# Kernel optimization log

Hardware: AMD Instinct MI355X
Metric: run time of the kernel (lower is better)

The kernel has to match this reference:

```python
import jax, jax.numpy as jnp
import numpy as np

NUM_CLASSES = 2
THRESHOLD = 0.5
NEGPOS_RATIO = 3
VAR0, VAR1 = 0.1, 0.2  # self.variance = [0.1, 0.2]


def point_form(priors):
    # [cx,cy,w,h] -> [xmin,ymin,xmax,ymax]
    return jnp.concatenate([priors[:, :2] - priors[:, 2:] / 2,
                            priors[:, :2] + priors[:, 2:] / 2], axis=1)


def jaccard(a, b):
    # a: [O,4], b: [P,4] point-form -> IoU [O,P]
    tl = jnp.maximum(a[:, None, :2], b[None, :, :2])
    br = jnp.minimum(a[:, None, 2:], b[None, :, 2:])
    wh = jnp.clip(br - tl, 0.0)
    inter = wh[..., 0] * wh[..., 1]
    area_a = ((a[:, 2] - a[:, 0]) * (a[:, 3] - a[:, 1]))[:, None]
    area_b = ((b[:, 2] - b[:, 0]) * (b[:, 3] - b[:, 1]))[None, :]
    return inter / (area_a + area_b - inter)


def encode(matched, priors):
    # matched: [P,4] point-form GT, priors: [P,4] center-size
    g_cxcy = ((matched[:, :2] + matched[:, 2:]) / 2 - priors[:, :2]) / (VAR0 * priors[:, 2:])
    g_wh = jnp.log((matched[:, 2:] - matched[:, :2]) / priors[:, 2:]) / VAR1
    return jnp.concatenate([g_cxcy, g_wh], axis=1)


def match_one(truths, labels, priors):
    # truths: [O,4], labels: [O], priors: [P,4]
    O = truths.shape[0]
    overlaps = jaccard(truths, point_form(priors))          # [O,P]
    best_prior_idx = jnp.argmax(overlaps, axis=1)           # [O] best prior per GT
    best_truth_overlap = jnp.max(overlaps, axis=0)          # [P]
    best_truth_idx = jnp.argmax(overlaps, axis=0)           # [P]
    # ensure each GT keeps its best prior
    best_truth_overlap = best_truth_overlap.at[best_prior_idx].set(2.0)
    best_truth_idx = best_truth_idx.at[best_prior_idx].set(jnp.arange(O))
    matches = truths[best_truth_idx]                        # [P,4]
    conf = labels[best_truth_idx].astype(jnp.int32)         # head label == 1
    conf = jnp.where(best_truth_overlap < THRESHOLD, 0, conf)
    loc = encode(matches, priors)                           # [P,4]
    return loc, conf


def setup_inputs() -> dict:
    key = jax.random.key(0)
    k1, k2, k3, k4, k5, k6 = jax.random.split(key, 6)
    B, P, O = 32, 32768, 32
    loc_data = jax.random.normal(k1, (B, P, 3), jnp.float32) * 0.1
    conf_data = jax.random.normal(k2, (B, P, 2), jnp.float32)
    cxy = jax.random.uniform(k3, (P, 2), jnp.float32, 0.1, 0.9)
    wh = jax.random.uniform(k4, (P, 2), jnp.float32, 0.05, 0.2)
    priors = jnp.concatenate([cxy, wh], axis=1)
    xy1 = jax.random.uniform(k5, (B, O, 2), jnp.float32, 0.0, 0.7)
    twh = jax.random.uniform(k6, (B, O, 2), jnp.float32, 0.05, 0.25)
    targets = jnp.concatenate([xy1, xy1 + twh, jnp.ones((B, O, 1), jnp.float32)], axis=2)
    return {"loc_data": loc_data, "conf_data": conf_data, "priors": priors, "targets": targets}


def reference(loc_data, conf_data, priors, targets):
    B, P, _ = loc_data.shape
    # convert_coord: [cx, cy, gw] -> [cx, cy, gw, gw]
    quard = jnp.stack([loc_data[..., 0], loc_data[..., 1],
                       loc_data[..., 2], loc_data[..., 2]], axis=-1)  # [B,P,4]
    truths = targets[..., :4]
    labels = targets[..., 4]
    loc_t, conf_t = jax.vmap(lambda t, l: match_one(t, l, priors))(truths, labels)
    pos = conf_t > 0                                         # [B,P]
    # localization smooth-L1 over positives (sum reduction)
    d = quard - loc_t
    ad = jnp.abs(d)
    sl1 = jnp.where(ad < 1.0, 0.5 * d * d, ad - 0.5)
    loss_l = jnp.sum(sl1 * pos[..., None].astype(sl1.dtype))
    # per-prior CE for hard-negative mining
    lse = jax.nn.logsumexp(conf_data, axis=-1)               # [B,P]
    picked = jnp.take_along_axis(conf_data, conf_t[..., None], axis=-1)[..., 0]
    ce = lse - picked                                        # [B,P]
    ce_mine = jnp.where(pos, 0.0, ce)
    # double argsort -> rank of each prior by mining loss (descending)
    loss_idx = jnp.argsort(-ce_mine, axis=1)
    idx_rank = jnp.argsort(loss_idx, axis=1)
    num_pos = jnp.sum(pos.astype(jnp.int32), axis=1, keepdims=True)  # [B,1]
    num_neg = jnp.minimum(NEGPOS_RATIO * num_pos, P - 1)
    neg = idx_rank < num_neg
    sel = jnp.logical_or(pos, neg)
    loss_c = jnp.sum(jnp.where(sel, ce, 0.0))
    N = jnp.sum(num_pos).astype(loss_l.dtype)
    return loss_l / N, loss_c / N
```

## Files before the change

### kernel.cpp

```cpp
#include <hip/hip_runtime.h>
#include <math.h>

#define Bn 32
#define Pn 32768
#define On 32
#define TPB 256
#define PPT 2
#define BP  (TPB * PPT)
#define AG 8
#define AC 1024


__device__ __forceinline__ unsigned long long shfl_down_u64(unsigned long long v, int off) {
    unsigned lo = (unsigned)(v & 0xFFFFFFFFull);
    unsigned hi = (unsigned)(v >> 32);
    lo = __shfl_down(lo, off, 64);
    hi = __shfl_down(hi, off, 64);
    return ((unsigned long long)hi << 32) | lo;
}

__global__ __launch_bounds__(256) void matchA(const float4* __restrict__ priors,
                                              const float* __restrict__ targets,
                                              unsigned long long* __restrict__ bpm) {
    int g    = blockIdx.x;
    int base = blockIdx.y * AC;
    int tid  = threadIdx.x;

    __shared__ float4 tb[AG];
    __shared__ float  ta[AG];
    __shared__ unsigned long long sbest[AG];

    if (tid < AG) {
        const float* t = targets + (size_t)(g * AG + tid) * 5;
        float x1 = t[0], y1 = t[1], x2 = t[2], y2 = t[3];
        tb[tid] = make_float4(x1, y1, x2, y2);
        ta[tid] = (x2 - x1) * (y2 - y1);
        sbest[tid] = 0ull;
    }
    __syncthreads();

    float px1[4], py1[4], px2[4], py2[4], ab[4];
#pragma unroll
    for (int j = 0; j < 4; j++) {
        float4 pr = priors[base + tid + 256 * j];
        px1[j] = pr.x - pr.z * 0.5f; py1[j] = pr.y - pr.w * 0.5f;
        px2[j] = pr.x + pr.z * 0.5f; py2[j] = pr.y + pr.w * 0.5f;
        ab[j]  = (px2[j] - px1[j]) * (py2[j] - py1[j]);
    }

#pragma unroll
    for (int o = 0; o < AG; o++) {
        float4 tt = tb[o];
        float  a  = ta[o];
        float bI = 0.f, bU = 1.f;
        int   bj = 0;
#pragma unroll
        for (int j = 0; j < 4; j++) {
            float ix1 = fmaxf(tt.x, px1[j]), iy1 = fmaxf(tt.y, py1[j]);
            float ix2 = fminf(tt.z, px2[j]), iy2 = fminf(tt.w, py2[j]);
            float iw = fmaxf(ix2 - ix1, 0.f), ih = fmaxf(iy2 - iy1, 0.f);
            float I = iw * ih;
            float U = a + ab[j] - I;
            if (I * bU > bI * U) { bI = I; bU = U; bj = j; }
        }
        int p = base + tid + 256 * bj;
        float iou = bI / bU;
        unsigned long long key = ((unsigned long long)__float_as_uint(iou) << 32)
                               | (unsigned)(Pn - 1 - p);
#pragma unroll
        for (int off = 32; off > 0; off >>= 1) {
            unsigned long long other = shfl_down_u64(key, off);
            if (other > key) key = other;
        }
        if ((tid & 63) == 0) atomicMax(&sbest[o], key);
    }
    __syncthreads();
    if (tid < AG) atomicMax(&bpm[g * AG + tid], sbest[tid]);
}

__global__ __launch_bounds__(256) void matchB(const float* __restrict__ loc,
                                              const float2* __restrict__ conf2,
                                              const float4* __restrict__ priors,
                                              const float* __restrict__ targets,
                                              const unsigned long long* __restrict__ bpm,
                                              float* __restrict__ ce_mine,
                                              int* __restrict__ num_pos,
                                              float* __restrict__ loss_l_t,
                                              float* __restrict__ ce_t,
                                              int* __restrict__ np_tot) {
    int b = blockIdx.y;
    int base = blockIdx.x * BP;
    int tid = threadIdx.x;

    __shared__ float4 tb[On];
    __shared__ float  ta[On], lb[On];
    __shared__ int    forced[BP];
    __shared__ float  sred[12];

#pragma unroll
    for (int j = 0; j < PPT; j++) forced[tid + 256 * j] = -1;
    int sp = -1;
    if (tid < On) {
        const float* t = targets + ((size_t)b * On + tid) * 5;
        float x1 = t[0], y1 = t[1], x2 = t[2], y2 = t[3];
        tb[tid] = make_float4(x1, y1, x2, y2);
        ta[tid] = (x2 - x1) * (y2 - y1);
        lb[tid] = t[4];
        sp = Pn - 1 - (int)(bpm[b * On + tid] & 0xFFFFFFFFull);
    }
    __syncthreads();
    if (tid < On && sp >= base && sp < base + BP)
        atomicMax(&forced[sp - base], tid);
    __syncthreads();

    float px1[PPT], py1[PPT], px2[PPT], py2[PPT], ab[PPT], pcx[PPT], pcy[PPT], pw[PPT], ph[PPT];
#pragma unroll
    for (int j = 0; j < PPT; j++) {
        float4 pr = priors[base + tid + 256 * j];
        pcx[j] = pr.x; pcy[j] = pr.y; pw[j] = pr.z; ph[j] = pr.w;
        px1[j] = pr.x - pr.z * 0.5f; py1[j] = pr.y - pr.w * 0.5f;
        px2[j] = pr.x + pr.z * 0.5f; py2[j] = pr.y + pr.w * 0.5f;
        ab[j]  = (px2[j] - px1[j]) * (py2[j] - py1[j]);
    }

    float bI[PPT] = {0.f, 0.f};
    float bU[PPT] = {1.f, 1.f};
    int   bx[PPT] = {0, 0};
#pragma unroll 4
    for (int o = 0; o < On; o++) {
        float4 tt = tb[o];
        float  a  = ta[o];
#pragma unroll
        for (int j = 0; j < PPT; j++) {
            float ix1 = fmaxf(tt.x, px1[j]), iy1 = fmaxf(tt.y, py1[j]);
            float ix2 = fminf(tt.z, px2[j]), iy2 = fminf(tt.w, py2[j]);
            float iw = fmaxf(ix2 - ix1, 0.f), ih = fmaxf(iy2 - iy1, 0.f);
            float I = iw * ih;
            float U = a + ab[j] - I;
            if (I * bU[j] > bI[j] * U) { bI[j] = I; bU[j] = U; bx[j] = o; }
        }
    }

    float ll_s = 0.f, pce_s = 0.f, cnt_s = 0.f;
#pragma unroll
    for (int j = 0; j < PPT; j++) {
        int p = base + tid + 256 * j;
        int fo = forced[tid + 256 * j];
        int bidx = (fo >= 0) ? fo : bx[j];
        int cf;
        if (fo >= 0)                      cf = (int)lb[bidx];
        else if (bI[j] >= 0.5f * bU[j])   cf = (int)lb[bidx];
        else                              cf = 0;
        bool pos = cf > 0;

        if (pos) {
            float4 tt = tb[bidx];
            float g0 = ((tt.x + tt.z) * 0.5f - pcx[j]) / (0.1f * pw[j]);
            float g1 = ((tt.y + tt.w) * 0.5f - pcy[j]) / (0.1f * ph[j]);
            float g2 = __logf((tt.z - tt.x) / pw[j]) * 5.0f;
            float g3 = __logf((tt.w - tt.y) / ph[j]) * 5.0f;
            const float* lp = loc + ((size_t)b * Pn + p) * 3;
            float q0 = lp[0], q1 = lp[1], q2 = lp[2];
            float dd[4] = { q0 - g0, q1 - g1, q2 - g2, q2 - g3 };
#pragma unroll
            for (int i = 0; i < 4; i++) {
                float ad = fabsf(dd[i]);
                ll_s += (ad < 1.f) ? 0.5f * dd[i] * dd[i] : (ad - 0.5f);
            }
            cnt_s += 1.f;
        }

        float2 cc = conf2[(size_t)b * Pn + p];
        float m = fmaxf(cc.x, cc.y);
        float lse = m + __logf(__expf(cc.x - m) + __expf(cc.y - m));
        float ce = lse - (cf ? cc.y : cc.x);
        if (pos) { pce_s += ce; ce = 0.f; }
        ce_mine[(size_t)b * Pn + p] = fmaxf(ce, 0.f);
    }

#pragma unroll
    for (int off = 32; off > 0; off >>= 1) {
        ll_s  += __shfl_down(ll_s,  off, 64);
        pce_s += __shfl_down(pce_s, off, 64);
        cnt_s += __shfl_down(cnt_s, off, 64);
    }
    int lane = tid & 63, wv = tid >> 6;
    if (lane == 0) { sred[wv * 3] = ll_s; sred[wv * 3 + 1] = pce_s; sred[wv * 3 + 2] = cnt_s; }
    __syncthreads();
    if (tid == 0) {
        float llr = 0, pcer = 0, cntr = 0;
        for (int w = 0; w < 4; w++) { llr += sred[w*3]; pcer += sred[w*3+1]; cntr += sred[w*3+2]; }
        if (llr != 0.f)  atomicAdd(loss_l_t, llr);
        if (pcer != 0.f) atomicAdd(ce_t, pcer);
        int c = (int)cntr;
        if (c) { atomicAdd(&num_pos[b], c); atomicAdd(np_tot, c); }
    }
}

__global__ __launch_bounds__(1024) void topk(const float* __restrict__ ce_mine,
                                             const int* __restrict__ num_pos,
                                             float* __restrict__ ce_t) {
    int b = blockIdx.x, tid = threadIdx.x;
    const float4* v4 = (const float4*)(ce_mine + (size_t)b * Pn);
    float4 r[8];
#pragma unroll
    for (int i = 0; i < 8; i++) r[i] = v4[i * 1024 + tid];

    int k = 3 * num_pos[b];
    if (k > Pn - 1) k = Pn - 1;
    if (k <= 0) return;

    __shared__ int hist[4][2048];
    __shared__ int wavetot[16];
    __shared__ int waveabove[16];
    __shared__ unsigned long long wcand[16];
    __shared__ unsigned s_lo;
    __shared__ int s_ab;
    __shared__ float ssum[16];
    __shared__ int   scnt[16];

    int lane = tid & 63, wv = tid >> 6;
    unsigned LO = 0u;
    int AB = 0;

    const int shifts[3] = {20, 9, 0};
    const int nbs[3]    = {2048, 2048, 512};

#pragma unroll
    for (int rd = 0; rd < 3; rd++) {
        int shift = shifts[rd], nb = nbs[rd];
        int* hf = &hist[0][0];
        for (int i = tid; i < 4 * 2048; i += 1024) hf[i] = 0;
        __syncthreads();
        int* myh = hist[wv >> 2];
#pragma unroll
        for (int i = 0; i < 8; i++) {
            float4 rv = r[i];
            float vals[4] = {rv.x, rv.y, rv.z, rv.w};
#pragma unroll
            for (int q = 0; q < 4; q++) {
                unsigned u = __float_as_uint(vals[q]);
                unsigned bin = (u - LO) >> shift;
                if (bin < (unsigned)nb) atomicAdd(&myh[bin], 1);
            }
        }
        __syncthreads();
        int c0 = hist[0][2*tid] + hist[1][2*tid] + hist[2][2*tid] + hist[3][2*tid];
        int c1 = hist[0][2*tid+1] + hist[1][2*tid+1] + hist[2][2*tid+1] + hist[3][2*tid+1];
        int local = c0 + c1;
        int suf = local;
#pragma unroll
        for (int off = 1; off < 64; off <<= 1) {
            int src = lane + off;
            int o = __shfl(suf, src & 63, 64);
            suf += (src < 64) ? o : 0;
        }
        if (lane == 0) wavetot[wv] = suf;
        __syncthreads();
        if (tid == 0) {
            int acc = AB;
            for (int w = 15; w >= 0; w--) { waveabove[w] = acc; acc += wavetot[w]; }
        }
        __syncthreads();
        int S0 = waveabove[wv] + suf;
        int S1 = S0 - c0;
        int cand = -1; unsigned nab = 0;
        if (S0 >= k) { cand = 2*tid;     nab = (unsigned)(S0 - c0); }
        if (S1 >= k) { cand = 2*tid + 1; nab = (unsigned)(S1 - c1); }
        unsigned long long pk = ((unsigned long long)(unsigned)(cand + 1) << 32) | nab;
#pragma unroll
        for (int off = 32; off > 0; off >>= 1) {
            unsigned long long o = shfl_down_u64(pk, off);
            if (o > pk) pk = o;
        }
        if (lane == 0) wcand[wv] = pk;
        __syncthreads();
        if (tid == 0) {
            unsigned long long best = 0;
            for (int w = 0; w < 16; w++) if (wcand[w] > best) best = wcand[w];
            int ci = (int)(best >> 32) - 1;
            s_lo = LO + ((unsigned)ci << shift);
            s_ab = (int)(best & 0xFFFFFFFFu);
        }
        __syncthreads();
        LO = s_lo; AB = s_ab;
    }
    float tau = __uint_as_float(LO);
    float s = 0.f; int c = 0;
#pragma unroll
    for (int i = 0; i < 8; i++) {
        if (r[i].x > tau) { s += r[i].x; c++; }
        if (r[i].y > tau) { s += r[i].y; c++; }
        if (r[i].z > tau) { s += r[i].z; c++; }
        if (r[i].w > tau) { s += r[i].w; c++; }
    }
#pragma unroll
    for (int off = 32; off > 0; off >>= 1) {
        s += __shfl_down(s, off, 64);
        c += __shfl_down(c, off, 64);
    }
    if (lane == 0) { ssum[wv] = s; scnt[wv] = c; }
    __syncthreads();
    if (tid == 0) {
        float st = 0.f; int ct = 0;
        for (int w = 0; w < 16; w++) { st += ssum[w]; ct += scnt[w]; }
        atomicAdd(ce_t, st + (float)(k - ct) * tau);
    }
}

__global__ void finalize(const float* __restrict__ loss_l_t,
                         const float* __restrict__ ce_t,
                         const int* __restrict__ np_tot,
                         float* __restrict__ out) {
    float N = (float)(*np_tot);
    out[0] = *loss_l_t / N;
    out[1] = *ce_t / N;
}

extern "C" void kernel_launch(void* const* d_in, const int* in_sizes, int n_in,
                              void* d_out, int out_size, void* d_ws, size_t ws_size,
                              hipStream_t stream) {
    const float* loc     = (const float*)d_in[0];
    const float* conf    = (const float*)d_in[1];
    const float* priors  = (const float*)d_in[2];
    const float* targets = (const float*)d_in[3];
    float* out = (float*)d_out;

    char* ws = (char*)d_ws;
    unsigned long long* bpm = (unsigned long long*)ws;
    int*   num_pos  = (int*)(ws + 8192);
    float* loss_l_t = (float*)(ws + 8320);
    float* ce_t     = (float*)(ws + 8324);
    int*   np_tot   = (int*)(ws + 8328);
    float* ce_mine  = (float*)(ws + 16384);

    hipMemsetAsync(ws, 0, 16384, stream);

    hipLaunchKernelGGL(matchA, dim3((Bn * On) / AG, Pn / AC), dim3(256), 0, stream,
                       (const float4*)priors, targets, bpm);
    hipLaunchKernelGGL(matchB, dim3(Pn / BP, Bn), dim3(256), 0, stream,
                       loc, (const float2*)conf, (const float4*)priors, targets, bpm,
                       ce_mine, num_pos, loss_l_t, ce_t, np_tot);
    hipLaunchKernelGGL(topk, dim3(Bn), dim3(1024), 0, stream, ce_mine, num_pos, ce_t);
    hipLaunchKernelGGL(finalize, dim3(1), dim3(1), 0, stream, loss_l_t, ce_t, np_tot, out);
}
```

Before: 195.2 us.

## Fuse finalize into topk via last-block ticket, widen matchB per-thread work

The separate finalize launch is removed. The last topk block to finish now computes the outputs, using an atomic ticket counter and a threadfence. matchB goes from 2 to 4 priors per thread, so it launches half as many blocks. Its confidence loads are issued early to overlap with the IoU loop, and the IoU scan over ground-truth boxes is split into two independent argmax chains to shorten the dependency chain, merged afterwards. The wider per-thread work raises register pressure, and halving the grid may reduce occupancy.

```diff
diff --git a/kernel.cpp b/kernel.cpp
--- a/kernel.cpp
+++ b/kernel.cpp
@@ -5,7 +5,7 @@
 #define Pn 32768
 #define On 32
 #define TPB 256
-#define PPT 2
+#define PPT 4
 #define BP  (TPB * PPT)
 #define AG 8
 #define AC 1024
@@ -92,6 +92,10 @@
     int base = blockIdx.x * BP;
     int tid = threadIdx.x;
 
+    float2 cc[PPT];
+#pragma unroll
+    for (int j = 0; j < PPT; j++) cc[j] = conf2[(size_t)b * Pn + base + tid + 256 * j];
+
     __shared__ float4 tb[On];
     __shared__ float  ta[On], lb[On];
     __shared__ int    forced[BP];
@@ -123,22 +127,37 @@
         ab[j]  = (px2[j] - px1[j]) * (py2[j] - py1[j]);
     }
 
-    float bI[PPT] = {0.f, 0.f};
-    float bU[PPT] = {1.f, 1.f};
-    int   bx[PPT] = {0, 0};
-#pragma unroll 4
-    for (int o = 0; o < On; o++) {
-        float4 tt = tb[o];
-        float  a  = ta[o];
-#pragma unroll
-        for (int j = 0; j < PPT; j++) {
-            float ix1 = fmaxf(tt.x, px1[j]), iy1 = fmaxf(tt.y, py1[j]);
-            float ix2 = fminf(tt.z, px2[j]), iy2 = fminf(tt.w, py2[j]);
-            float iw = fmaxf(ix2 - ix1, 0.f), ih = fmaxf(iy2 - iy1, 0.f);
-            float I = iw * ih;
-            float U = a + ab[j] - I;
-            if (I * bU[j] > bI[j] * U) { bI[j] = I; bU[j] = U; bx[j] = o; }
-        }
+    float bIc[PPT][2], bUc[PPT][2];
+    int   bxc[PPT][2];
+#pragma unroll
+    for (int j = 0; j < PPT; j++)
+#pragma unroll
+        for (int h = 0; h < 2; h++) { bIc[j][h] = 0.f; bUc[j][h] = 1.f; bxc[j][h] = h * 16; }
+
+#pragma unroll 2
+    for (int o16 = 0; o16 < 16; o16++) {
+#pragma unroll
+        for (int h = 0; h < 2; h++) {
+            int o = h * 16 + o16;
+            float4 tt = tb[o];
+            float  a  = ta[o];
+#pragma unroll
+            for (int j = 0; j < PPT; j++) {
+                float ix1 = fmaxf(tt.x, px1[j]), iy1 = fmaxf(tt.y, py1[j]);
+                float ix2 = fminf(tt.z, px2[j]), iy2 = fminf(tt.w, py2[j]);
+                float iw = fmaxf(ix2 - ix1, 0.f), ih = fmaxf(iy2 - iy1, 0.f);
+                float I = iw * ih;
+                float U = a + ab[j] - I;
+                if (I * bUc[j][h] > bIc[j][h] * U) { bIc[j][h] = I; bUc[j][h] = U; bxc[j][h] = o; }
+            }
+        }
+    }
+    float bI[PPT], bU[PPT];
+    int   bx[PPT];
+#pragma unroll
+    for (int j = 0; j < PPT; j++) {
+        bI[j] = bIc[j][0]; bU[j] = bUc[j][0]; bx[j] = bxc[j][0];
+        if (bIc[j][1] * bU[j] > bI[j] * bUc[j][1]) { bI[j] = bIc[j][1]; bU[j] = bUc[j][1]; bx[j] = bxc[j][1]; }
     }
 
     float ll_s = 0.f, pce_s = 0.f, cnt_s = 0.f;
@@ -170,10 +189,9 @@
             cnt_s += 1.f;
         }
 
-        float2 cc = conf2[(size_t)b * Pn + p];
-        float m = fmaxf(cc.x, cc.y);
-        float lse = m + __logf(__expf(cc.x - m) + __expf(cc.y - m));
-        float ce = lse - (cf ? cc.y : cc.x);
+        float m = fmaxf(cc[j].x, cc[j].y);
+        float lse = m + __logf(__expf(cc[j].x - m) + __expf(cc[j].y - m));
+        float ce = lse - (cf ? cc[j].y : cc[j].x);
         if (pos) { pce_s += ce; ce = 0.f; }
         ce_mine[(size_t)b * Pn + p] = fmaxf(ce, 0.f);
     }
@@ -199,7 +217,11 @@
 
 __global__ __launch_bounds__(1024) void topk(const float* __restrict__ ce_mine,
                                              const int* __restrict__ num_pos,
-                                             float* __restrict__ ce_t) {
+                                             float* __restrict__ ce_t,
+                                             const float* __restrict__ loss_l_t,
+                                             const int* __restrict__ np_tot,
+                                             unsigned* __restrict__ tick,
+                                             float* __restrict__ out) {
     int b = blockIdx.x, tid = threadIdx.x;
     const float4* v4 = (const float4*)(ce_mine + (size_t)b * Pn);
     float4 r[8];
@@ -208,7 +230,6 @@
 
     int k = 3 * num_pos[b];
     if (k > Pn - 1) k = Pn - 1;
-    if (k <= 0) return;
 
     __shared__ int hist[4][2048];
     __shared__ int wavetot[16];
@@ -220,101 +241,107 @@
     __shared__ int   scnt[16];
 
     int lane = tid & 63, wv = tid >> 6;
-    unsigned LO = 0u;
-    int AB = 0;
-
-    const int shifts[3] = {20, 9, 0};
-    const int nbs[3]    = {2048, 2048, 512};
-
-#pragma unroll
-    for (int rd = 0; rd < 3; rd++) {
-        int shift = shifts[rd], nb = nbs[rd];
-        int* hf = &hist[0][0];
-        for (int i = tid; i < 4 * 2048; i += 1024) hf[i] = 0;
-        __syncthreads();
-        int* myh = hist[wv >> 2];
+
+    if (k > 0) {
+        unsigned LO = 0u;
+        int AB = 0;
+
+        const int shifts[3] = {20, 9, 0};
+        const int nbs[3]    = {2048, 2048, 512};
+
+#pragma unroll
+        for (int rd = 0; rd < 3; rd++) {
+            int shift = shifts[rd], nb = nbs[rd];
+            int* hf = &hist[0][0];
+            for (int i = tid; i < 4 * 2048; i += 1024) hf[i] = 0;
+            __syncthreads();
+            int* myh = hist[wv >> 2];
+#pragma unroll
+            for (int i = 0; i < 8; i++) {
+                float4 rv = r[i];
+                float vals[4] = {rv.x, rv.y, rv.z, rv.w};
+#pragma unroll
+                for (int q = 0; q < 4; q++) {
+                    unsigned u = __float_as_uint(vals[q]);
+                    unsigned bin = (u - LO) >> shift;
+                    if (bin < (unsigned)nb) atomicAdd(&myh[bin], 1);
+                }
+            }
+            __syncthreads();
+            int c0 = hist[0][2*tid] + hist[1][2*tid] + hist[2][2*tid] + hist[3][2*tid];
+            int c1 = hist[0][2*tid+1] + hist[1][2*tid+1] + hist[2][2*tid+1] + hist[3][2*tid+1];
+            int local = c0 + c1;
+            int suf = local;
+#pragma unroll
+            for (int off = 1; off < 64; off <<= 1) {
+                int src = lane + off;
+                int o = __shfl(suf, src & 63, 64);
+                suf += (src < 64) ? o : 0;
+            }
+            if (lane == 0) wavetot[wv] = suf;
+            __syncthreads();
+            if (tid == 0) {
+                int acc = AB;
+                for (int w = 15; w >= 0; w--) { waveabove[w] = acc; acc += wavetot[w]; }
+            }
+            __syncthreads();
+            int S0 = waveabove[wv] + suf;
+            int S1 = S0 - c0;
+            int cand = -1; unsigned nab = 0;
+            if (S0 >= k) { cand = 2*tid;     nab = (unsigned)(S0 - c0); }
+            if (S1 >= k) { cand = 2*tid + 1; nab = (unsigned)(S1 - c1); }
+            unsigned long long pk = ((unsigned long long)(unsigned)(cand + 1) << 32) | nab;
+#pragma unroll
+            for (int off = 32; off > 0; off >>= 1) {
+                unsigned long long o = shfl_down_u64(pk, off);
+                if (o > pk) pk = o;
+            }
+            if (lane == 0) wcand[wv] = pk;
+            __syncthreads();
+            if (tid == 0) {
+                unsigned long long best = 0;
+                for (int w = 0; w < 16; w++) if (wcand[w] > best) best = wcand[w];
+                int ci = (int)(best >> 32) - 1;
+                s_lo = LO + ((unsigned)ci << shift);
+                s_ab = (int)(best & 0xFFFFFFFFu);
+            }
+            __syncthreads();
+            LO = s_lo; AB = s_ab;
+        }
+        float tau = __uint_as_float(LO);
+        float s = 0.f; int c = 0;
 #pragma unroll
         for (int i = 0; i < 8; i++) {
-            float4 rv = r[i];
-            float vals[4] = {rv.x, rv.y, rv.z, rv.w};
-#pragma unroll
-            for (int q = 0; q < 4; q++) {
-                unsigned u = __float_as_uint(vals[q]);
-                unsigned bin = (u - LO) >> shift;
-                if (bin < (unsigned)nb) atomicAdd(&myh[bin], 1);
-            }
-        }
-        __syncthreads();
-        int c0 = hist[0][2*tid] + hist[1][2*tid] + hist[2][2*tid] + hist[3][2*tid];
-        int c1 = hist[0][2*tid+1] + hist[1][2*tid+1] + hist[2][2*tid+1] + hist[3][2*tid+1];
-        int local = c0 + c1;
-        int suf = local;
-#pragma unroll
-        for (int off = 1; off < 64; off <<= 1) {
-            int src = lane + off;
-            int o = __shfl(suf, src & 63, 64);
-            suf += (src < 64) ? o : 0;
-        }
-        if (lane == 0) wavetot[wv] = suf;
+            if (r[i].x > tau) { s += r[i].x; c++; }
+            if (r[i].y > tau) { s += r[i].y; c++; }
+            if (r[i].z > tau) { s += r[i].z; c++; }
+            if (r[i].w > tau) { s += r[i].w; c++; }
+        }
+#pragma unroll
+        for (int off = 32; off > 0; off >>= 1) {
+            s += __shfl_down(s, off, 64);
+            c += __shfl_down(c, off, 64);
+        }
+        if (lane == 0) { ssum[wv] = s; scnt[wv] = c; }
         __syncthreads();
         if (tid == 0) {
-            int acc = AB;
-            for (int w = 15; w >= 0; w--) { waveabove[w] = acc; acc += wavetot[w]; }
-        }
-        __syncthreads();
-        int S0 = waveabove[wv] + suf;
-        int S1 = S0 - c0;
-        int cand = -1; unsigned nab = 0;
-        if (S0 >= k) { cand = 2*tid;     nab = (unsigned)(S0 - c0); }
-        if (S1 >= k) { cand = 2*tid + 1; nab = (unsigned)(S1 - c1); }
-        unsigned long long pk = ((unsigned long long)(unsigned)(cand + 1) << 32) | nab;
-#pragma unroll
-        for (int off = 32; off > 0; off >>= 1) {
-            unsigned long long o = shfl_down_u64(pk, off);
-            if (o > pk) pk = o;
-        }
-        if (lane == 0) wcand[wv] = pk;
-        __syncthreads();
-        if (tid == 0) {
-            unsigned long long best = 0;
-            for (int w = 0; w < 16; w++) if (wcand[w] > best) best = wcand[w];
-            int ci = (int)(best >> 32) - 1;
-            s_lo = LO + ((unsigned)ci << shift);
-            s_ab = (int)(best & 0xFFFFFFFFu);
-        }
-        __syncthreads();
-        LO = s_lo; AB = s_ab;
-    }
-    float tau = __uint_as_float(LO);
-    float s = 0.f; int c = 0;
-#pragma unroll
-    for (int i = 0; i < 8; i++) {
-        if (r[i].x > tau) { s += r[i].x; c++; }
-        if (r[i].y > tau) { s += r[i].y; c++; }
-        if (r[i].z > tau) { s += r[i].z; c++; }
-        if (r[i].w > tau) { s += r[i].w; c++; }
-    }
-#pragma unroll
-    for (int off = 32; off > 0; off >>= 1) {
-        s += __shfl_down(s, off, 64);
-        c += __shfl_down(c, off, 64);
-    }
-    if (lane == 0) { ssum[wv] = s; scnt[wv] = c; }
-    __syncthreads();
+            float st = 0.f; int ct = 0;
+            for (int w = 0; w < 16; w++) { st += ssum[w]; ct += scnt[w]; }
+            atomicAdd(ce_t, st + (float)(k - ct) * tau);
+        }
+    }
+
     if (tid == 0) {
-        float st = 0.f; int ct = 0;
-        for (int w = 0; w < 16; w++) { st += ssum[w]; ct += scnt[w]; }
-        atomicAdd(ce_t, st + (float)(k - ct) * tau);
-    }
-}
-
-__global__ void finalize(const float* __restrict__ loss_l_t,
-                         const float* __restrict__ ce_t,
-                         const int* __restrict__ np_tot,
-                         float* __restrict__ out) {
-    float N = (float)(*np_tot);
-    out[0] = *loss_l_t / N;
-    out[1] = *ce_t / N;
+        __threadfence();
+        unsigned done = atomicAdd(tick, 1u);
+        if (done == (unsigned)(Bn - 1)) {
+            float N  = (float)atomicAdd((int*)np_tot, 0);
+            float ll = atomicAdd((float*)loss_l_t, 0.f);
+            float ce = atomicAdd(ce_t, 0.f);
+            out[0] = ll / N;
+            out[1] = ce / N;
+        }
+    }
 }
 
 extern "C" void kernel_launch(void* const* d_in, const int* in_sizes, int n_in,
@@ -332,6 +359,7 @@
     float* loss_l_t = (float*)(ws + 8320);
     float* ce_t     = (float*)(ws + 8324);
     int*   np_tot   = (int*)(ws + 8328);
+    unsigned* tick  = (unsigned*)(ws + 8332);
     float* ce_mine  = (float*)(ws + 16384);
 
     hipMemsetAsync(ws, 0, 16384, stream);
@@ -341,6 +369,6 @@
     hipLaunchKernelGGL(matchB, dim3(Pn / BP, Bn), dim3(256), 0, stream,
                        loc, (const float2*)conf, (const float4*)priors, targets, bpm,
                        ce_mine, num_pos, loss_l_t, ce_t, np_tot);
-    hipLaunchKernelGGL(topk, dim3(Bn), dim3(1024), 0, stream, ce_mine, num_pos, ce_t);
-    hipLaunchKernelGGL(finalize, dim3(1), dim3(1), 0, stream, loss_l_t, ce_t, np_tot, out);
-}
+    hipLaunchKernelGGL(topk, dim3(Bn), dim3(1024), 0, stream,
+                       ce_mine, num_pos, ce_t, loss_l_t, np_tot, tick, out);
+}
```

New measurement: 157.7 us. 19.2% less time.
